# Kernel optimization log

Measured on AMD Instinct MI355X. Metric: run time of the kernel, lower is better.

Reference implementation:

```python
import jax, jax.numpy as jnp
import numpy as np
from jax import lax

B, L, D = 2, 1024, 1024
INTER = 2816  # _find_multiple(round(4.0*1024*2/3), 256)
K, PAD = 3, 1
S = 32  # sqrt(L)
K2 = K * K


def setup_inputs() -> dict:
    key = jax.random.key(0)
    ks = jax.random.split(key, 7)
    x = jax.random.normal(ks[0], (B, L, D), dtype=jnp.float32)
    w_gate_up = jax.random.normal(ks[1], (2 * INTER, D), dtype=jnp.float32) / np.sqrt(D)
    w_metric = jax.random.normal(ks[2], (7, INTER, 3, 3), dtype=jnp.float32) / np.sqrt(INTER * 9)
    b_metric = jax.random.normal(ks[3], (7,), dtype=jnp.float32) * 0.01
    conv_w = jax.random.normal(ks[4], (INTER, 1, K, K), dtype=jnp.float32) / K
    conv_b = jnp.zeros((INTER,), dtype=jnp.float32)
    w_down = jax.random.normal(ks[5], (D, INTER), dtype=jnp.float32) / np.sqrt(INTER)
    return {"x": x, "w_gate_up": w_gate_up, "w_metric": w_metric,
            "b_metric": b_metric, "conv_w": conv_w, "conv_b": conv_b,
            "w_down": w_down}


def _metric_offsets(x2d, w_metric, b_metric):
    # Finsler-Randers style metric: 2x2 linear map M, drift vector, tanh scale.
    p = lax.conv_general_dilated(x2d, w_metric, (1, 1), 'SAME',
                                 dimension_numbers=('NCHW', 'OIHW', 'NCHW'))
    p = p + b_metric[None, :, None, None]  # [B,7,S,S]
    m00, m01, m10, m11 = p[:, 0], p[:, 1], p[:, 2], p[:, 3]
    dr_y, dr_x = p[:, 4], p[:, 5]
    scale = jnp.tanh(p[:, 6])
    ky = (jnp.arange(K) - PAD).astype(x2d.dtype)
    py = jnp.repeat(ky, K)   # (K2,) kernel-tap dy
    px = jnp.tile(ky, K)     # (K2,) kernel-tap dx
    pyb = py[None, :, None, None]
    pxb = px[None, :, None, None]
    off_y = scale[:, None] * (m00[:, None] * pyb + m01[:, None] * pxb) + dr_y[:, None]
    off_x = scale[:, None] * (m10[:, None] * pyb + m11[:, None] * pxb) + dr_x[:, None]
    return off_y, off_x, py, px  # offsets: [B,K2,S,S]


def _deform_depthwise(x2d, off_y, off_x, py, px, conv_w, conv_b):
    # Sampling positions per output pixel & kernel tap: [B,K2,S,S]
    iy = jnp.arange(S, dtype=x2d.dtype)
    pos_y = iy[None, None, :, None] + py[None, :, None, None] + off_y
    pos_x = iy[None, None, None, :] + px[None, :, None, None] + off_x
    y0 = jnp.floor(pos_y)
    x0 = jnp.floor(pos_x)
    ty = pos_y - y0
    tx = pos_x - x0
    y0i = y0.astype(jnp.int32)
    x0i = x0.astype(jnp.int32)
    flat = x2d.reshape(B, INTER, S * S)

    def corner(yy, xx):
        valid = ((yy >= 0) & (yy < S) & (xx >= 0) & (xx < S)).astype(x2d.dtype)
        idx = (jnp.clip(yy, 0, S - 1) * S + jnp.clip(xx, 0, S - 1)).reshape(B, 1, -1)
        v = jnp.take_along_axis(flat, idx, axis=2).reshape(B, INTER, K2, S, S)
        return v * valid[:, None]

    w00 = ((1 - ty) * (1 - tx))[:, None]
    w01 = ((1 - ty) * tx)[:, None]
    w10 = (ty * (1 - tx))[:, None]
    w11 = (ty * tx)[:, None]
    acc = w00 * corner(y0i, x0i)
    acc = acc + w01 * corner(y0i, x0i + 1)
    acc = acc + w10 * corner(y0i + 1, x0i)
    acc = acc + w11 * corner(y0i + 1, x0i + 1)
    out = jnp.einsum('bckij,ck->bcij', acc, conv_w.reshape(INTER, K2))
    return out + conv_b[None, :, None, None]


def reference(x, w_gate_up, w_metric, b_metric, conv_w, conv_b, w_down):
    gu = jnp.einsum('bld,fd->blf', x, w_gate_up)          # [B,L,2*inter]
    gate, up = jnp.split(gu, 2, axis=-1)
    x_ffn = jax.nn.silu(gate) * up                         # [B,L,inter]
    x2d = x_ffn.transpose(0, 2, 1).reshape(B, INTER, S, S)
    off_y, off_x, py, px = _metric_offsets(x2d, w_metric, b_metric)
    out2d = _deform_depthwise(x2d, off_y, off_x, py, px, conv_w, conv_b)
    grid_out = out2d.reshape(B, INTER, L).transpose(0, 2, 1)
    return jnp.einsum('blf,df->bld', grid_out, w_down)
```

## Files before the change

kernel.cpp:

```cpp
#include <hip/hip_runtime.h>
#include <hip/hip_bf16.h>
#include <cstdint>
#include <cstddef>
#include <type_traits>

#define INTER 2816

typedef __bf16 bf16x8 __attribute__((ext_vector_type(8)));
typedef float f32x4 __attribute__((ext_vector_type(4)));
typedef unsigned short u16x8 __attribute__((ext_vector_type(8)));
using bf16 = __hip_bfloat16;
using u16 = unsigned short;

__device__ __forceinline__ u16 f2bu(float f) {
  bf16 h = __float2bfloat16(f);
  return *reinterpret_cast<u16*>(&h);
}
__device__ __forceinline__ float bu2f(u16 u) {
  bf16 h = *reinterpret_cast<bf16*>(&u);
  return __bfloat162float(h);
}

__device__ __forceinline__ void async16(const u16* g, u16* l) {
  __builtin_amdgcn_global_load_lds(
      (const __attribute__((address_space(1))) unsigned int*)g,
      (__attribute__((address_space(3))) unsigned int*)l, 16, 0, 0);
}

__device__ __forceinline__ void stage8(u16* dst, const float* src) {
  const float4 a = *(const float4*)(src);
  const float4 b = *(const float4*)(src + 4);
  u16 tmp[8] = {f2bu(a.x), f2bu(a.y), f2bu(a.z), f2bu(a.w),
                f2bu(b.x), f2bu(b.y), f2bu(b.z), f2bu(b.w)};
  *(uint4*)dst = *(uint4*)tmp;
}

__global__ __launch_bounds__(256)
void prep_all(const float* __restrict__ x, const float* __restrict__ wgu,
              const float* __restrict__ wd, const float* __restrict__ w_metric,
              const float* __restrict__ conv_w, u16* __restrict__ xbf,
              u16* __restrict__ wgubf, u16* __restrict__ wdbf,
              u16* __restrict__ wm2, float* __restrict__ cwT) {
  constexpr size_t S0 = (size_t)2048 * 1024;
  constexpr size_t S1 = (size_t)5632 * 1024;
  constexpr size_t S2 = (size_t)1024 * 2816;
  constexpr size_t NCONV_THREADS = (S0 + S1 + S2) / 8;
  const size_t t = (size_t)blockIdx.x * 256 + threadIdx.x;
  if (t < NCONV_THREADS) {
    const size_t e0 = t * 8;
    const float* src;
    u16* dst;
    size_t off;
    if (e0 < S0) {
      src = x; dst = xbf; off = e0;
    } else if (e0 < S0 + S1) {
      src = wgu; dst = wgubf; off = e0 - S0;
    } else {
      src = wd; dst = wdbf; off = e0 - S0 - S1;
    }
    stage8(dst + off, src + off);
  } else {
    const unsigned p = (unsigned)(t - NCONV_THREADS);
    const unsigned y = p / 2816u;
    const unsigned c = p - y * 2816u;
    if (y < 128) {
      float v = 0.f;
      if (y < 63) {
        const unsigned o = y / 9, tap = y - o * 9;
        v = w_metric[((size_t)o * INTER + c) * 9 + tap];
      }
      wm2[(size_t)y * INTER + c] = f2bu(v);
    } else {
      const unsigned k = y - 128;
      cwT[(size_t)k * INTER + c] = conv_w[(size_t)c * 9 + k];
    }
  }
}

template <typename OT>
__global__ __launch_bounds__(256, 3)
void gemm_nt(const u16* __restrict__ A, int lda, const u16* __restrict__ Bt,
             int ldb, OT* __restrict__ C, int M, int ldc, int K) {
  __shared__ u16 As[2][128 * 32];
  __shared__ u16 Bs[2][128 * 32];
  const size_t koff = (size_t)blockIdx.z * K;
  A += koff;
  Bt += koff;
  C += (size_t)blockIdx.z * M * ldc;
  const int m0 = blockIdx.x * 128;
  const int n0 = blockIdx.y * 128;
  const int tid = threadIdx.x;
  const int lane = tid & 63;
  const int wv = tid >> 6;
  const int wm = wv & 1, wn = wv >> 1;
  const int lr = lane & 15;
  const int lq = lane >> 4;

  f32x4 acc[4][4];
#pragma unroll
  for (int i = 0; i < 4; ++i)
#pragma unroll
    for (int j = 0; j < 4; ++j) acc[i][j] = (f32x4){0.f, 0.f, 0.f, 0.f};

  const int srow = tid >> 2;
  const int scol = (tid & 3) * 8;
  const u16* gA0 = A + (size_t)(m0 + srow) * lda + scol;
  const u16* gA1 = A + (size_t)(m0 + 64 + srow) * lda + scol;
  const u16* gB0 = Bt + (size_t)(n0 + srow) * ldb + scol;
  const u16* gB1 = Bt + (size_t)(n0 + 64 + srow) * ldb + scol;

  const int nIter = K >> 5;
  async16(gA0, &As[0][tid * 8]);
  async16(gA1, &As[0][2048 + tid * 8]);
  async16(gB0, &Bs[0][tid * 8]);
  async16(gB1, &Bs[0][2048 + tid * 8]);

  for (int it = 0; it < nIter; ++it) {
    __syncthreads();
    const int cur = it & 1;
    const u16* as = As[cur];
    const u16* bs = Bs[cur];
    if (it + 1 < nIter) {
      const int kb = (it + 1) << 5;
      const int nxt = cur ^ 1;
      async16(gA0 + kb, &As[nxt][tid * 8]);
      async16(gA1 + kb, &As[nxt][2048 + tid * 8]);
      async16(gB0 + kb, &Bs[nxt][tid * 8]);
      async16(gB1 + kb, &Bs[nxt][2048 + tid * 8]);
    }
    bf16x8 af[4], bfr[4];
#pragma unroll
    for (int i = 0; i < 4; ++i)
      af[i] = *(const bf16x8*)(&as[(wm * 64 + i * 16 + lr) * 32 + lq * 8]);
#pragma unroll
    for (int j = 0; j < 4; ++j)
      bfr[j] = *(const bf16x8*)(&bs[(wn * 64 + j * 16 + lr) * 32 + lq * 8]);
#pragma unroll
    for (int i = 0; i < 4; ++i)
#pragma unroll
      for (int j = 0; j < 4; ++j)
        acc[i][j] = __builtin_amdgcn_mfma_f32_16x16x32_bf16(af[i], bfr[j],
                                                            acc[i][j], 0, 0, 0);
  }

#pragma unroll
  for (int i = 0; i < 4; ++i)
#pragma unroll
    for (int j = 0; j < 4; ++j) {
      const int col = n0 + wn * 64 + j * 16 + lr;
#pragma unroll
      for (int r = 0; r < 4; ++r) {
        const int row = m0 + wm * 64 + i * 16 + lq * 4 + r;
        const float v = acc[i][j][r];
        if constexpr (std::is_same_v<OT, float>) {
          C[(size_t)row * ldc + col] = v;
        } else {
          C[(size_t)row * ldc + col] = f2bu(v);
        }
      }
    }
}

__global__ void reduce4(const float* __restrict__ q2, float* __restrict__ out) {
  const size_t i = ((size_t)blockIdx.x * 256 + threadIdx.x) * 4;
  const size_t S = (size_t)2048 * 1024;
  float4 a = *(const float4*)(q2 + i);
  const float4 b = *(const float4*)(q2 + S + i);
  const float4 c = *(const float4*)(q2 + 2 * S + i);
  const float4 d = *(const float4*)(q2 + 3 * S + i);
  a.x += b.x + c.x + d.x;
  a.y += b.y + c.y + d.y;
  a.z += b.z + c.z + d.z;
  a.w += b.w + c.w + d.w;
  *(float4*)(out + i) = a;
}

__global__ __launch_bounds__(256, 2)
void gateup_gemm(const u16* __restrict__ x, const u16* __restrict__ wgu,
                 u16* __restrict__ xffn) {
  constexpr int K = 1024;
  __shared__ u16 As[2][128 * 32];
  __shared__ u16 Bgs[2][64 * 32];
  __shared__ u16 Bus[2][64 * 32];
  const int m0 = blockIdx.x * 128;
  const int n0 = blockIdx.y * 64;
  const int tid = threadIdx.x;
  const int lane = tid & 63;
  const int wv = tid >> 6;
  const int wm = wv & 1, wn = wv >> 1;
  const int lr = lane & 15;
  const int lq = lane >> 4;

  f32x4 accg[4][2], accu[4][2];
#pragma unroll
  for (int i = 0; i < 4; ++i)
#pragma unroll
    for (int j = 0; j < 2; ++j) {
      accg[i][j] = (f32x4){0.f, 0.f, 0.f, 0.f};
      accu[i][j] = (f32x4){0.f, 0.f, 0.f, 0.f};
    }

  const int srow = tid >> 2;
  const int scol = (tid & 3) * 8;
  const u16* gA0 = x + (size_t)(m0 + srow) * K + scol;
  const u16* gA1 = x + (size_t)(m0 + 64 + srow) * K + scol;
  const u16* gBg = wgu + (size_t)(n0 + srow) * K + scol;
  const u16* gBu = wgu + (size_t)(INTER + n0 + srow) * K + scol;

  constexpr int nIter = K >> 5;
  async16(gA0, &As[0][tid * 8]);
  async16(gA1, &As[0][2048 + tid * 8]);
  async16(gBg, &Bgs[0][tid * 8]);
  async16(gBu, &Bus[0][tid * 8]);

  for (int it = 0; it < nIter; ++it) {
    __syncthreads();
    const int cur = it & 1;
    const u16* as = As[cur];
    const u16* bgs = Bgs[cur];
    const u16* bus = Bus[cur];
    if (it + 1 < nIter) {
      const int kb = (it + 1) << 5;
      const int nxt = cur ^ 1;
      async16(gA0 + kb, &As[nxt][tid * 8]);
      async16(gA1 + kb, &As[nxt][2048 + tid * 8]);
      async16(gBg + kb, &Bgs[nxt][tid * 8]);
      async16(gBu + kb, &Bus[nxt][tid * 8]);
    }
    bf16x8 af[4], bg[2], bu[2];
#pragma unroll
    for (int i = 0; i < 4; ++i)
      af[i] = *(const bf16x8*)(&as[(wm * 64 + i * 16 + lr) * 32 + lq * 8]);
#pragma unroll
    for (int j = 0; j < 2; ++j) {
      bg[j] = *(const bf16x8*)(&bgs[(wn * 32 + j * 16 + lr) * 32 + lq * 8]);
      bu[j] = *(const bf16x8*)(&bus[(wn * 32 + j * 16 + lr) * 32 + lq * 8]);
    }
#pragma unroll
    for (int i = 0; i < 4; ++i)
#pragma unroll
      for (int j = 0; j < 2; ++j) {
        accg[i][j] = __builtin_amdgcn_mfma_f32_16x16x32_bf16(af[i], bg[j],
                                                             accg[i][j], 0, 0, 0);
        accu[i][j] = __builtin_amdgcn_mfma_f32_16x16x32_bf16(af[i], bu[j],
                                                             accu[i][j], 0, 0, 0);
      }
  }

#pragma unroll
  for (int i = 0; i < 4; ++i)
#pragma unroll
    for (int j = 0; j < 2; ++j) {
      const int col = n0 + wn * 32 + j * 16 + lr;
#pragma unroll
      for (int r = 0; r < 4; ++r) {
        const int row = m0 + wm * 64 + i * 16 + lq * 4 + r;
        const float g = accg[i][j][r];
        const float u = accu[i][j][r];
        const float s = g / (1.f + __expf(-g));
        xffn[(size_t)row * INTER + col] = f2bu(s * u);
      }
    }
}

__global__ __launch_bounds__(64)
void offsets_fused(const float* __restrict__ q,
                   const float* __restrict__ b_metric,
                   int4* __restrict__ samp) {
  __shared__ float lds[130 * 65];
  const int chunk = blockIdx.x;
  const int b = chunk >> 4;
  const int c0 = (chunk & 15) * 64;
  const int t = threadIdx.x;

  for (int v = t; v < 130 * 16; v += 64) {
    const int row = v >> 4;
    const int c4 = (v & 15) * 4;
    int pg = c0 - 33 + row;
    pg = min(max(pg, 0), 1023);
    const float* src = q + ((size_t)b * 1024 + pg) * 128 + c4;
    float4 s = *(const float4*)(src);
#pragma unroll
    for (int ks = 1; ks < 8; ++ks) {
      const float4 vv = *(const float4*)(src + (size_t)ks * 2048 * 128);
      s.x += vv.x; s.y += vv.y; s.z += vv.z; s.w += vv.w;
    }
    float* d = &lds[row * 65 + c4];
    d[0] = s.x; d[1] = s.y; d[2] = s.z; d[3] = s.w;
  }
  __syncthreads();

  const int pix = c0 + t;
  const int i = pix >> 5, j = pix & 31;
  float p[7];
#pragma unroll
  for (int o = 0; o < 7; ++o) p[o] = b_metric[o];
#pragma unroll
  for (int tap = 0; tap < 9; ++tap) {
    const int dy = tap / 3 - 1, dx = tap % 3 - 1;
    const int ii = i + dy, jj = j + dx;
    if ((unsigned)ii < 32u && (unsigned)jj < 32u) {
      const float* r = &lds[(t + 33 + dy * 32 + dx) * 65 + tap];
#pragma unroll
      for (int o = 0; o < 7; ++o) p[o] += r[o * 9];
    }
  }
  const float m00 = p[0], m01 = p[1], m10 = p[2], m11 = p[3];
  const float dry = p[4], drx = p[5];
  const float sc = tanhf(p[6]);
#pragma unroll
  for (int k = 0; k < 9; ++k) {
    const float pyk = (float)(k / 3 - 1), pxk = (float)(k % 3 - 1);
    const float offy = sc * (m00 * pyk + m01 * pxk) + dry;
    const float offx = sc * (m10 * pyk + m11 * pxk) + drx;
    const float posy = (float)i + pyk + offy;
    const float posx = (float)j + pxk + offx;
    const float y0f = floorf(posy), x0f = floorf(posx);
    int4 s;
    s.x = (int)y0f;
    s.y = (int)x0f;
    s.z = __float_as_int(posy - y0f);
    s.w = __float_as_int(posx - x0f);
    samp[((size_t)b * 9 + k) * 1024 + pix] = s;
  }
}

__global__ __launch_bounds__(256)
void deform_kernel(const u16* __restrict__ xffn,
                   const int4* __restrict__ samp,
                   const float* __restrict__ cwT,
                   const float* __restrict__ conv_b,
                   u16* __restrict__ gridout) {
  const unsigned t = blockIdx.x * 256 + threadIdx.x;
  const unsigned pix = t / 352u;
  const unsigned cv = t - pix * 352u;
  const int c0 = cv * 8;
  const int b = pix >> 10, l = pix & 1023;

  float acc[8];
  {
    const float4 b0 = *(const float4*)(&conv_b[c0]);
    const float4 b1 = *(const float4*)(&conv_b[c0 + 4]);
    acc[0] = b0.x; acc[1] = b0.y; acc[2] = b0.z; acc[3] = b0.w;
    acc[4] = b1.x; acc[5] = b1.y; acc[6] = b1.z; acc[7] = b1.w;
  }
  const size_t pixbase = (size_t)b * 1024;
#pragma unroll
  for (int k = 0; k < 9; ++k) {
    const int4 s = samp[((size_t)b * 9 + k) * 1024 + l];
    const int y0 = s.x, x0 = s.y;
    const float ty = __int_as_float(s.z), tx = __int_as_float(s.w);
    const int y1 = y0 + 1, x1 = x0 + 1;
    const float vy0 = ((unsigned)y0 < 32u) ? 1.f : 0.f;
    const float vy1 = ((unsigned)y1 < 32u) ? 1.f : 0.f;
    const float vx0 = ((unsigned)x0 < 32u) ? 1.f : 0.f;
    const float vx1 = ((unsigned)x1 < 32u) ? 1.f : 0.f;
    const float w00 = (1.f - ty) * (1.f - tx) * vy0 * vx0;
    const float w01 = (1.f - ty) * tx * vy0 * vx1;
    const float w10 = ty * (1.f - tx) * vy1 * vx0;
    const float w11 = ty * tx * vy1 * vx1;
    const int cy0 = min(max(y0, 0), 31), cy1 = min(max(y1, 0), 31);
    const int cx0 = min(max(x0, 0), 31), cx1 = min(max(x1, 0), 31);
    const u16x8 v00 = *(const u16x8*)(&xffn[(pixbase + cy0 * 32 + cx0) * INTER + c0]);
    const u16x8 v01 = *(const u16x8*)(&xffn[(pixbase + cy0 * 32 + cx1) * INTER + c0]);
    const u16x8 v10 = *(const u16x8*)(&xffn[(pixbase + cy1 * 32 + cx0) * INTER + c0]);
    const u16x8 v11 = *(const u16x8*)(&xffn[(pixbase + cy1 * 32 + cx1) * INTER + c0]);
    const float4 cwa = *(const float4*)(&cwT[(size_t)k * INTER + c0]);
    const float4 cwb = *(const float4*)(&cwT[(size_t)k * INTER + c0 + 4]);
    const float cw[8] = {cwa.x, cwa.y, cwa.z, cwa.w, cwb.x, cwb.y, cwb.z, cwb.w};
#pragma unroll
    for (int e = 0; e < 8; ++e) {
      const float bl = w00 * bu2f(v00[e]) + w01 * bu2f(v01[e]) +
                       w10 * bu2f(v10[e]) + w11 * bu2f(v11[e]);
      acc[e] += bl * cw[e];
    }
  }
  u16 outv[8];
#pragma unroll
  for (int e = 0; e < 8; ++e) outv[e] = f2bu(acc[e]);
  *(uint4*)(&gridout[(pixbase + l) * INTER + c0]) = *(uint4*)outv;
}

extern "C" void kernel_launch(void* const* d_in, const int* in_sizes, int n_in,
                              void* d_out, int out_size, void* d_ws,
                              size_t ws_size, hipStream_t stream) {
  const float* x         = (const float*)d_in[0];
  const float* w_gate_up = (const float*)d_in[1];
  const float* w_metric  = (const float*)d_in[2];
  const float* b_metric  = (const float*)d_in[3];
  const float* conv_w    = (const float*)d_in[4];
  const float* conv_b    = (const float*)d_in[5];
  const float* w_down    = (const float*)d_in[6];
  float* out = (float*)d_out;

  char* w = (char*)d_ws;
  u16* gridout  = (u16*)(w);
  float* q2     = (float*)(w + (12u << 20));
  u16* xffn     = (u16*)(w + (12u << 20));
  u16* xbf      = (u16*)(w + (24u << 20));
  u16* wgubf    = (u16*)(w + (28u << 20) + (256u << 10));
  float* q_conv = (float*)(w + (28u << 20) + (256u << 10));
  u16* wm2      = (u16*)(w + (40u << 20));
  float* cwT    = (float*)(w + (41u << 20));
  int4* samp    = (int4*)(w + (42u << 20));
  u16* wdbf     = (u16*)(w + (44u << 20));

  prep_all<<<6755, 256, 0, stream>>>(x, w_gate_up, w_down, w_metric, conv_w,
                                     xbf, wgubf, wdbf, wm2, cwT);
  gateup_gemm<<<dim3(16, 44), 256, 0, stream>>>(xbf, wgubf, xffn);
  gemm_nt<float><<<dim3(16, 1, 8), 256, 0, stream>>>(
      xffn, INTER, wm2, INTER, q_conv, 2048, 128, 352);
  offsets_fused<<<32, 64, 0, stream>>>(q_conv, b_metric, samp);
  deform_kernel<<<2816, 256, 0, stream>>>(xffn, samp, cwT, conv_b, gridout);
  gemm_nt<float><<<dim3(16, 8, 4), 256, 0, stream>>>(
      gridout, INTER, wdbf, INTER, q2, 2048, 1024, 704);
  reduce4<<<2048, 256, 0, stream>>>(q2, out);
}
```

Before: 212.0 us.

## Precompute bilinear weights and offsets; widen deform kernel to 16 channels per thread

The offsets kernel now emits ready-to-use bilinear weights (validity masks folded in) and clamped byte offsets, so the deform kernel no longer recomputes them per thread. Each deform thread handles 16 channels instead of 8, which halves the grid and the per-thread loads of sampling records. Depthwise conv weights are stored as bf16 to cut their traffic. The gate-up GEMM grid is transposed so consecutive blocks walk along N, which changes L2 reuse order. Costs are more registers per thread, a small precision loss in the conv weights, and double the record storage.

```diff
diff --git a/kernel.cpp b/kernel.cpp
--- a/kernel.cpp
+++ b/kernel.cpp
@@ -40,7 +40,7 @@
               const float* __restrict__ wd, const float* __restrict__ w_metric,
               const float* __restrict__ conv_w, u16* __restrict__ xbf,
               u16* __restrict__ wgubf, u16* __restrict__ wdbf,
-              u16* __restrict__ wm2, float* __restrict__ cwT) {
+              u16* __restrict__ wm2, u16* __restrict__ cwb) {
   constexpr size_t S0 = (size_t)2048 * 1024;
   constexpr size_t S1 = (size_t)5632 * 1024;
   constexpr size_t S2 = (size_t)1024 * 2816;
@@ -72,7 +72,7 @@
       wm2[(size_t)y * INTER + c] = f2bu(v);
     } else {
       const unsigned k = y - 128;
-      cwT[(size_t)k * INTER + c] = conv_w[(size_t)c * 9 + k];
+      cwb[(size_t)k * INTER + c] = f2bu(conv_w[(size_t)c * 9 + k]);
     }
   }
 }
@@ -182,8 +182,8 @@
   __shared__ u16 As[2][128 * 32];
   __shared__ u16 Bgs[2][64 * 32];
   __shared__ u16 Bus[2][64 * 32];
-  const int m0 = blockIdx.x * 128;
-  const int n0 = blockIdx.y * 64;
+  const int n0 = blockIdx.x * 64;
+  const int m0 = blockIdx.y * 128;
   const int tid = threadIdx.x;
   const int lane = tid & 63;
   const int wv = tid >> 6;
@@ -266,7 +266,7 @@
 __global__ __launch_bounds__(64)
 void offsets_fused(const float* __restrict__ q,
                    const float* __restrict__ b_metric,
-                   int4* __restrict__ samp) {
+                   float4* __restrict__ wrec, int4* __restrict__ orec) {
   __shared__ float lds[130 * 65];
   const int chunk = blockIdx.x;
   const int b = chunk >> 4;
@@ -316,69 +316,83 @@
     const float posy = (float)i + pyk + offy;
     const float posx = (float)j + pxk + offx;
     const float y0f = floorf(posy), x0f = floorf(posx);
-    int4 s;
-    s.x = (int)y0f;
-    s.y = (int)x0f;
-    s.z = __float_as_int(posy - y0f);
-    s.w = __float_as_int(posx - x0f);
-    samp[((size_t)b * 9 + k) * 1024 + pix] = s;
-  }
-}
-
-__global__ __launch_bounds__(256)
-void deform_kernel(const u16* __restrict__ xffn,
-                   const int4* __restrict__ samp,
-                   const float* __restrict__ cwT,
-                   const float* __restrict__ conv_b,
-                   u16* __restrict__ gridout) {
-  const unsigned t = blockIdx.x * 256 + threadIdx.x;
-  const unsigned pix = t / 352u;
-  const unsigned cv = t - pix * 352u;
-  const int c0 = cv * 8;
-  const int b = pix >> 10, l = pix & 1023;
-
-  float acc[8];
-  {
-    const float4 b0 = *(const float4*)(&conv_b[c0]);
-    const float4 b1 = *(const float4*)(&conv_b[c0 + 4]);
-    acc[0] = b0.x; acc[1] = b0.y; acc[2] = b0.z; acc[3] = b0.w;
-    acc[4] = b1.x; acc[5] = b1.y; acc[6] = b1.z; acc[7] = b1.w;
-  }
-  const size_t pixbase = (size_t)b * 1024;
-#pragma unroll
-  for (int k = 0; k < 9; ++k) {
-    const int4 s = samp[((size_t)b * 9 + k) * 1024 + l];
-    const int y0 = s.x, x0 = s.y;
-    const float ty = __int_as_float(s.z), tx = __int_as_float(s.w);
+    const int y0 = (int)y0f, x0 = (int)x0f;
+    const float ty = posy - y0f, tx = posx - x0f;
     const int y1 = y0 + 1, x1 = x0 + 1;
     const float vy0 = ((unsigned)y0 < 32u) ? 1.f : 0.f;
     const float vy1 = ((unsigned)y1 < 32u) ? 1.f : 0.f;
     const float vx0 = ((unsigned)x0 < 32u) ? 1.f : 0.f;
     const float vx1 = ((unsigned)x1 < 32u) ? 1.f : 0.f;
-    const float w00 = (1.f - ty) * (1.f - tx) * vy0 * vx0;
-    const float w01 = (1.f - ty) * tx * vy0 * vx1;
-    const float w10 = ty * (1.f - tx) * vy1 * vx0;
-    const float w11 = ty * tx * vy1 * vx1;
+    float4 w;
+    w.x = (1.f - ty) * (1.f - tx) * vy0 * vx0;
+    w.y = (1.f - ty) * tx * vy0 * vx1;
+    w.z = ty * (1.f - tx) * vy1 * vx0;
+    w.w = ty * tx * vy1 * vx1;
     const int cy0 = min(max(y0, 0), 31), cy1 = min(max(y1, 0), 31);
     const int cx0 = min(max(x0, 0), 31), cx1 = min(max(x1, 0), 31);
-    const u16x8 v00 = *(const u16x8*)(&xffn[(pixbase + cy0 * 32 + cx0) * INTER + c0]);
-    const u16x8 v01 = *(const u16x8*)(&xffn[(pixbase + cy0 * 32 + cx1) * INTER + c0]);
-    const u16x8 v10 = *(const u16x8*)(&xffn[(pixbase + cy1 * 32 + cx0) * INTER + c0]);
-    const u16x8 v11 = *(const u16x8*)(&xffn[(pixbase + cy1 * 32 + cx1) * INTER + c0]);
-    const float4 cwa = *(const float4*)(&cwT[(size_t)k * INTER + c0]);
-    const float4 cwb = *(const float4*)(&cwT[(size_t)k * INTER + c0 + 4]);
-    const float cw[8] = {cwa.x, cwa.y, cwa.z, cwa.w, cwb.x, cwb.y, cwb.z, cwb.w};
+    int4 o;
+    o.x = (cy0 * 32 + cx0) * (INTER * 2);
+    o.y = (cy0 * 32 + cx1) * (INTER * 2);
+    o.z = (cy1 * 32 + cx0) * (INTER * 2);
+    o.w = (cy1 * 32 + cx1) * (INTER * 2);
+    const size_t r = (((size_t)b * 9 + k) << 10) + pix;
+    wrec[r] = w;
+    orec[r] = o;
+  }
+}
+
+__global__ __launch_bounds__(256)
+void deform_kernel(const u16* __restrict__ xffn,
+                   const float4* __restrict__ wrec,
+                   const int4* __restrict__ orec,
+                   const u16* __restrict__ cwb,
+                   const float* __restrict__ conv_b,
+                   u16* __restrict__ gridout) {
+  const unsigned t = blockIdx.x * 256 + threadIdx.x;
+  const unsigned pix = t / 176u;
+  const unsigned cv = t - pix * 176u;
+  const int c0 = cv * 16;
+  const int b = pix >> 10, l = pix & 1023;
+
+  float acc[16];
+#pragma unroll
+  for (int e = 0; e < 16; e += 4) {
+    const float4 bb = *(const float4*)(&conv_b[c0 + e]);
+    acc[e] = bb.x; acc[e + 1] = bb.y; acc[e + 2] = bb.z; acc[e + 3] = bb.w;
+  }
+  const char* xb = (const char*)xffn +
+                   ((size_t)b * 1024 * INTER + c0) * sizeof(u16);
+#pragma unroll
+  for (int k = 0; k < 9; ++k) {
+    const size_t r = (((size_t)b * 9 + k) << 10) + l;
+    const float4 w = wrec[r];
+    const int4 o = orec[r];
+    const u16x8 v00a = *(const u16x8*)(xb + o.x);
+    const u16x8 v00b = *(const u16x8*)(xb + o.x + 16);
+    const u16x8 v01a = *(const u16x8*)(xb + o.y);
+    const u16x8 v01b = *(const u16x8*)(xb + o.y + 16);
+    const u16x8 v10a = *(const u16x8*)(xb + o.z);
+    const u16x8 v10b = *(const u16x8*)(xb + o.z + 16);
+    const u16x8 v11a = *(const u16x8*)(xb + o.w);
+    const u16x8 v11b = *(const u16x8*)(xb + o.w + 16);
+    const u16x8 cwa = *(const u16x8*)(&cwb[(size_t)k * INTER + c0]);
+    const u16x8 cwbv = *(const u16x8*)(&cwb[(size_t)k * INTER + c0 + 8]);
 #pragma unroll
     for (int e = 0; e < 8; ++e) {
-      const float bl = w00 * bu2f(v00[e]) + w01 * bu2f(v01[e]) +
-                       w10 * bu2f(v10[e]) + w11 * bu2f(v11[e]);
-      acc[e] += bl * cw[e];
-    }
-  }
-  u16 outv[8];
-#pragma unroll
-  for (int e = 0; e < 8; ++e) outv[e] = f2bu(acc[e]);
-  *(uint4*)(&gridout[(pixbase + l) * INTER + c0]) = *(uint4*)outv;
+      const float bl = w.x * bu2f(v00a[e]) + w.y * bu2f(v01a[e]) +
+                       w.z * bu2f(v10a[e]) + w.w * bu2f(v11a[e]);
+      acc[e] += bl * bu2f(cwa[e]);
+      const float bl2 = w.x * bu2f(v00b[e]) + w.y * bu2f(v01b[e]) +
+                        w.z * bu2f(v10b[e]) + w.w * bu2f(v11b[e]);
+      acc[8 + e] += bl2 * bu2f(cwbv[e]);
+    }
+  }
+  u16 outv[16];
+#pragma unroll
+  for (int e = 0; e < 16; ++e) outv[e] = f2bu(acc[e]);
+  u16* dst = gridout + ((size_t)b * 1024 + l) * INTER + c0;
+  *(uint4*)(dst) = *(uint4*)(outv);
+  *(uint4*)(dst + 8) = *(uint4*)(outv + 8);
 }
 
 extern "C" void kernel_launch(void* const* d_in, const int* in_sizes, int n_in,
@@ -401,17 +415,19 @@
   u16* wgubf    = (u16*)(w + (28u << 20) + (256u << 10));
   float* q_conv = (float*)(w + (28u << 20) + (256u << 10));
   u16* wm2      = (u16*)(w + (40u << 20));
-  float* cwT    = (float*)(w + (41u << 20));
-  int4* samp    = (int4*)(w + (42u << 20));
+  u16* cwb      = (u16*)(w + (41u << 20));
+  float4* wrec  = (float4*)(w + (42u << 20));
+  int4* orec    = (int4*)(w + (43u << 20));
   u16* wdbf     = (u16*)(w + (44u << 20));
 
   prep_all<<<6755, 256, 0, stream>>>(x, w_gate_up, w_down, w_metric, conv_w,
-                                     xbf, wgubf, wdbf, wm2, cwT);
-  gateup_gemm<<<dim3(16, 44), 256, 0, stream>>>(xbf, wgubf, xffn);
+                                     xbf, wgubf, wdbf, wm2, cwb);
+  gateup_gemm<<<dim3(44, 16), 256, 0, stream>>>(xbf, wgubf, xffn);
   gemm_nt<float><<<dim3(16, 1, 8), 256, 0, stream>>>(
       xffn, INTER, wm2, INTER, q_conv, 2048, 128, 352);
-  offsets_fused<<<32, 64, 0, stream>>>(q_conv, b_metric, samp);
-  deform_kernel<<<2816, 256, 0, stream>>>(xffn, samp, cwT, conv_b, gridout);
+  offsets_fused<<<32, 64, 0, stream>>>(q_conv, b_metric, wrec, orec);
+  deform_kernel<<<1408, 256, 0, stream>>>(xffn, wrec, orec, cwb, conv_b,
+                                          gridout);
   gemm_nt<float><<<dim3(16, 8, 4), 256, 0, stream>>>(
       gridout, INTER, wdbf, INTER, q2, 2048, 1024, 704);
   reduce4<<<2048, 256, 0, stream>>>(q2, out);
```

Measured after the change: 231.6 us. +9.2%, slower.
